# Kernel optimization log

Hardware: AMD Instinct MI355X
Metric: run time of the kernel (lower is better)

The kernel has to match this reference:

```python
import jax, jax.numpy as jnp
import numpy as np

N = 50000
E = 800000
D_IN = 256
D_OUT = 256
ALPHA = 0.5


def setup_inputs() -> dict:
    key = jax.random.key(0)
    k1, k2, k3, k4, k5, k6 = jax.random.split(key, 6)
    stdv = 1.0 / np.sqrt(D_OUT)
    return {
        "input": jax.random.normal(k1, (N, D_IN), dtype=jnp.float32),
        "adj_src": jax.random.randint(k2, (E,), 0, N, dtype=jnp.int64),
        "adj_dst": jax.random.randint(k3, (E,), 0, N, dtype=jnp.int64),
        "adj_w": jax.random.uniform(k4, (E,), dtype=jnp.float32),
        "init_input": jax.random.normal(k5, (N, D_OUT), dtype=jnp.float32),
        "weight": jax.random.uniform(k6, (D_IN, D_OUT), dtype=jnp.float32,
                                     minval=-stdv, maxval=stdv),
    }


def reference(input, adj_src, adj_dst, adj_w, init_input, weight):
    # support = input @ W          [N, D_OUT] (dense GEMM)
    support = jnp.matmul(input, weight)
    # spmm: out[dst] += w * support[src]   (COO aggregate)
    msgs = support[adj_src] * adj_w[:, None]          # [E, D_OUT]
    agg = jax.ops.segment_sum(msgs, adj_dst, num_segments=N)  # [N, D_OUT]
    # alpha-blended residual + ReLU (bias=False, act=ReLU)
    out = agg * ALPHA + init_input * (1.0 - ALPHA)
    return jax.nn.relu(out)
```

## Files before the change

kernel.cpp:

```cpp
#include <hip/hip_runtime.h>
#include <hip/hip_fp16.h>

#define ALPHA 0.5f

typedef short short8v __attribute__((ext_vector_type(8)));
typedef float f32x4 __attribute__((ext_vector_type(4)));

__device__ __forceinline__ unsigned short f2bf(float f) {
  union { float f; unsigned u; } v; v.f = f;
  unsigned r = v.u + 0x7FFFu + ((v.u >> 16) & 1u);
  return (unsigned short)(r >> 16);
}
__device__ __forceinline__ float bf2f(unsigned short u) {
  union { unsigned u; float f; } v; v.u = ((unsigned)u) << 16;
  return v.f;
}

__global__ void transpose_w(const float* __restrict__ W, unsigned short* __restrict__ Wt) {
  __shared__ float tile[16][17];
  int kb = blockIdx.x * 16, nb = blockIdx.y * 16;
  tile[threadIdx.y][threadIdx.x] = W[(kb + threadIdx.y) * 256 + nb + threadIdx.x];
  __syncthreads();
  Wt[(nb + threadIdx.y) * 256 + kb + threadIdx.x] = f2bf(tile[threadIdx.x][threadIdx.y]);
}

__global__ __launch_bounds__(256) void gemm_mfma(
    const float* __restrict__ A, const unsigned short* __restrict__ Wt,
    unsigned short* __restrict__ C, int M) {
  __shared__ char smem[2][24576];
  const int tid = threadIdx.x;
  const int lane = tid & 63;
  const int w = tid >> 6;
  const int wm = w >> 1, wn = w & 1;
  const int row0 = blockIdx.x * 128;

  f32x4 acc[4][8];
  #pragma unroll
  for (int m = 0; m < 4; ++m)
    #pragma unroll
    for (int n = 0; n < 8; ++n) acc[m][n] = (f32x4){0.f, 0.f, 0.f, 0.f};

  const int aR = tid >> 1;
  const int aKs = (tid & 1) * 16;
  const int aRow = (row0 + aR < M) ? (row0 + aR) : (M - 1);
  const float* aP = A + (size_t)aRow * 256 + aKs;
  const int aWrOff = (aR >> 4) * 1024 + (aKs >> 3) * 256 + (aR & 15) * 16;

  int cur = 0;
  {
    float4 av[4];
    #pragma unroll
    for (int j = 0; j < 4; ++j) av[j] = *reinterpret_cast<const float4*>(aP + j * 4);
    #pragma unroll
    for (int i = 0; i < 4; ++i) {
      int s = w * 4 + i;
      const unsigned short* g = Wt + (size_t)(s * 16 + (lane & 15)) * 256 + (lane >> 4) * 8;
      __builtin_amdgcn_global_load_lds(
          (const __attribute__((address_space(1))) void*)g,
          (__attribute__((address_space(3))) void*)(&smem[0][8192 + s * 1024]),
          16, 0, 0);
    }
    unsigned short ab[16];
    #pragma unroll
    for (int j = 0; j < 4; ++j) {
      ab[j * 4 + 0] = f2bf(av[j].x); ab[j * 4 + 1] = f2bf(av[j].y);
      ab[j * 4 + 2] = f2bf(av[j].z); ab[j * 4 + 3] = f2bf(av[j].w);
    }
    *reinterpret_cast<short8v*>(&smem[0][aWrOff])       = *reinterpret_cast<short8v*>(&ab[0]);
    *reinterpret_cast<short8v*>(&smem[0][aWrOff + 256]) = *reinterpret_cast<short8v*>(&ab[8]);
    __syncthreads();
  }

  #pragma unroll
  for (int t = 0; t < 8; ++t) {
    float4 av[4];
    const bool pf = (t < 7);
    if (pf) {
      const int k0 = (t + 1) * 32;
      #pragma unroll
      for (int j = 0; j < 4; ++j) av[j] = *reinterpret_cast<const float4*>(aP + k0 + j * 4);
      #pragma unroll
      for (int i = 0; i < 4; ++i) {
        int s = w * 4 + i;
        const unsigned short* g = Wt + (size_t)(s * 16 + (lane & 15)) * 256 + k0 + (lane >> 4) * 8;
        __builtin_amdgcn_global_load_lds(
            (const __attribute__((address_space(1))) void*)g,
            (__attribute__((address_space(3))) void*)(&smem[cur ^ 1][8192 + s * 1024]),
            16, 0, 0);
      }
    }
    short8v af[4], bfv[8];
    #pragma unroll
    for (int m = 0; m < 4; ++m)
      af[m] = *reinterpret_cast<const short8v*>(&smem[cur][(wm * 4 + m) * 1024 + lane * 16]);
    #pragma unroll
    for (int n = 0; n < 8; ++n)
      bfv[n] = *reinterpret_cast<const short8v*>(&smem[cur][8192 + (wn * 8 + n) * 1024 + lane * 16]);
    #pragma unroll
    for (int m = 0; m < 4; ++m)
      #pragma unroll
      for (int n = 0; n < 8; ++n)
        acc[m][n] = __builtin_amdgcn_mfma_f32_16x16x32_bf16(af[m], bfv[n], acc[m][n], 0, 0, 0);
    if (pf) {
      unsigned short ab[16];
      #pragma unroll
      for (int j = 0; j < 4; ++j) {
        ab[j * 4 + 0] = f2bf(av[j].x); ab[j * 4 + 1] = f2bf(av[j].y);
        ab[j * 4 + 2] = f2bf(av[j].z); ab[j * 4 + 3] = f2bf(av[j].w);
      }
      *reinterpret_cast<short8v*>(&smem[cur ^ 1][aWrOff])       = *reinterpret_cast<short8v*>(&ab[0]);
      *reinterpret_cast<short8v*>(&smem[cur ^ 1][aWrOff + 256]) = *reinterpret_cast<short8v*>(&ab[8]);
    }
    __syncthreads();
    cur ^= 1;
  }

  #pragma unroll
  for (int m = 0; m < 4; ++m) {
    #pragma unroll
    for (int n = 0; n < 8; ++n) {
      const int col = wn * 128 + n * 16 + (lane & 15);
      #pragma unroll
      for (int r = 0; r < 4; ++r) {
        const int row = row0 + wm * 64 + m * 16 + (lane >> 4) * 4 + r;
        if (row < M) C[(size_t)row * 256 + col] = f2bf(acc[m][n][r]);
      }
    }
  }
}

__global__ void histogram_dst(const int* __restrict__ dst, int* __restrict__ deg, int E) {
  int i = blockIdx.x * blockDim.x + threadIdx.x;
  if (i < E) atomicAdd(&deg[dst[i]], 1);
}

__global__ __launch_bounds__(256) void scan_pass1(const int* __restrict__ deg,
                                                  int* __restrict__ excl,
                                                  int* __restrict__ partial, int N) {
  const int tid = threadIdx.x;
  const int base = blockIdx.x * 1024 + tid * 4;
  int4 v = make_int4(0, 0, 0, 0);
  if (base + 3 < N) v = *reinterpret_cast<const int4*>(&deg[base]);
  else {
    if (base + 0 < N) v.x = deg[base + 0];
    if (base + 1 < N) v.y = deg[base + 1];
    if (base + 2 < N) v.z = deg[base + 2];
  }
  const int s = v.x + v.y + v.z + v.w;
  const int lane = tid & 63, wid = tid >> 6;
  int ps = s;
  #pragma unroll
  for (int off = 1; off < 64; off <<= 1) {
    int t = __shfl_up(ps, off, 64);
    if (lane >= off) ps += t;
  }
  __shared__ int wsum[4];
  if (lane == 63) wsum[wid] = ps;
  __syncthreads();
  int woff = 0;
  #pragma unroll
  for (int w2 = 0; w2 < 4; ++w2) woff += (w2 < wid) ? wsum[w2] : 0;
  const int texcl = woff + ps - s;
  int4 e = make_int4(texcl, texcl + v.x, texcl + v.x + v.y, texcl + v.x + v.y + v.z);
  if (base + 3 < N) *reinterpret_cast<int4*>(&excl[base]) = e;
  else {
    if (base + 0 < N) excl[base + 0] = e.x;
    if (base + 1 < N) excl[base + 1] = e.y;
    if (base + 2 < N) excl[base + 2] = e.z;
  }
  if (tid == 255) partial[blockIdx.x] = woff + ps;
}

__global__ __launch_bounds__(256) void scan_pass2(const int* __restrict__ excl,
                                                  const int* __restrict__ partial,
                                                  int* __restrict__ row_ptr,
                                                  int* __restrict__ cursor, int N, int NB) {
  __shared__ int s_off;
  const int tid = threadIdx.x;
  if (tid < 64) {
    int v = (tid < NB && tid < (int)blockIdx.x) ? partial[tid] : 0;
    #pragma unroll
    for (int off = 1; off < 64; off <<= 1) v += __shfl_xor(v, off, 64);
    if (tid == 0) s_off = v;
  }
  __syncthreads();
  const int off = s_off;
  const int base = blockIdx.x * 1024 + tid * 4;
  if (base + 3 < N) {
    int4 v = *reinterpret_cast<const int4*>(&excl[base]);
    v.x += off; v.y += off; v.z += off; v.w += off;
    *reinterpret_cast<int4*>(&row_ptr[base]) = v;
    *reinterpret_cast<int4*>(&cursor[base]) = v;
  } else {
    for (int j = 0; j < 4; ++j)
      if (base + j < N) { int v = excl[base + j] + off; row_ptr[base + j] = v; cursor[base + j] = v; }
  }
}

__global__ void reindex_edges(const int* __restrict__ src, const int* __restrict__ dst,
                              const float* __restrict__ w, int* __restrict__ cursor,
                              unsigned* __restrict__ edges, int E) {
  int i = blockIdx.x * blockDim.x + threadIdx.x;
  if (i < E) {
    int d = dst[i];
    int slot = atomicAdd(&cursor[d], 1);
    unsigned hb = __half_as_ushort(__float2half(w[i] * ALPHA));
    edges[slot] = ((unsigned)src[i] << 15) | (hb >> 1);
  }
}

__device__ __forceinline__ float unpack_w(unsigned p) {
  return __half2float(__ushort_as_half((unsigned short)((p & 0x7FFFu) << 1)));
}

__global__ __launch_bounds__(256) void aggregate(
    const unsigned short* __restrict__ support,
    const int* __restrict__ row_ptr, const int* __restrict__ deg,
    const unsigned* __restrict__ edges,
    const float* __restrict__ init, float* __restrict__ out, int N) {
  int node = blockIdx.x * 4 + (threadIdx.x >> 6);
  if (node >= N) return;
  int lane = threadIdx.x & 63;
  int start = row_ptr[node], cnt = deg[node];

  float4 ini = *reinterpret_cast<const float4*>(&init[(size_t)node * 256 + lane * 4]);

  float4 acc = make_float4(0.f, 0.f, 0.f, 0.f);
  int e = 0;
  for (; e + 7 < cnt; e += 8) {
    unsigned p[8];
    #pragma unroll
    for (int j = 0; j < 8; ++j) p[j] = edges[start + e + j];
    ushort4 v[8];
    #pragma unroll
    for (int j = 0; j < 8; ++j)
      v[j] = *reinterpret_cast<const ushort4*>(&support[(size_t)(p[j] >> 15) * 256 + lane * 4]);
    #pragma unroll
    for (int j = 0; j < 8; ++j) {
      float wj = unpack_w(p[j]);
      acc.x += wj * bf2f(v[j].x);
      acc.y += wj * bf2f(v[j].y);
      acc.z += wj * bf2f(v[j].z);
      acc.w += wj * bf2f(v[j].w);
    }
  }
  for (; e < cnt; ++e) {
    unsigned p = edges[start + e];
    ushort4 v = *reinterpret_cast<const ushort4*>(&support[(size_t)(p >> 15) * 256 + lane * 4]);
    float wj = unpack_w(p);
    acc.x += wj * bf2f(v.x); acc.y += wj * bf2f(v.y);
    acc.z += wj * bf2f(v.z); acc.w += wj * bf2f(v.w);
  }
  float4 o;
  o.x = fmaxf(acc.x + (1.f - ALPHA) * ini.x, 0.f);
  o.y = fmaxf(acc.y + (1.f - ALPHA) * ini.y, 0.f);
  o.z = fmaxf(acc.z + (1.f - ALPHA) * ini.z, 0.f);
  o.w = fmaxf(acc.w + (1.f - ALPHA) * ini.w, 0.f);
  *reinterpret_cast<float4*>(&out[(size_t)node * 256 + lane * 4]) = o;
}

extern "C" void kernel_launch(void* const* d_in, const int* in_sizes, int n_in,
                              void* d_out, int out_size, void* d_ws, size_t ws_size,
                              hipStream_t stream) {
  const float* input   = (const float*)d_in[0];
  const int*   adj_src = (const int*)d_in[1];
  const int*   adj_dst = (const int*)d_in[2];
  const float* adj_w   = (const float*)d_in[3];
  const float* init_in = (const float*)d_in[4];
  const float* weight  = (const float*)d_in[5];
  float* out = (float*)d_out;

  const int N = in_sizes[0] / 256;
  const int E = in_sizes[1];

  char* ws = (char*)d_ws;
  unsigned short* support = (unsigned short*)ws; ws += (size_t)N * 256 * 2;
  unsigned short* Wt      = (unsigned short*)ws; ws += 256 * 256 * 2;
  int* deg     = (int*)ws; ws += (size_t)N * 4;
  int* row_ptr = (int*)ws; ws += (size_t)N * 4;
  int* cursor  = (int*)ws; ws += (size_t)N * 4;
  int* excl    = (int*)ws; ws += (size_t)N * 4;
  int* partial = (int*)ws; ws += 256;
  unsigned* edges = (unsigned*)ws; ws += (size_t)E * 4;

  const int NB = (N + 1023) / 1024;

  transpose_w<<<dim3(16, 16), dim3(16, 16), 0, stream>>>(weight, Wt);
  gemm_mfma<<<dim3((N + 127) / 128), 256, 0, stream>>>(input, Wt, support, N);

  hipMemsetAsync(deg, 0, (size_t)N * 4, stream);
  histogram_dst<<<(E + 255) / 256, 256, 0, stream>>>(adj_dst, deg, E);
  scan_pass1<<<NB, 256, 0, stream>>>(deg, excl, partial, N);
  scan_pass2<<<NB, 256, 0, stream>>>(excl, partial, row_ptr, cursor, N, NB);
  reindex_edges<<<(E + 255) / 256, 256, 0, stream>>>(adj_src, adj_dst, adj_w, cursor, edges, E);

  aggregate<<<(N + 3) / 4, 256, 0, stream>>>(support, row_ptr, deg, edges, init_in, out, N);
}
```

Before: 191.8 us.

## Store support in column slices and split aggregation across eight feature slices

The GEMM now writes support as eight column slices of 32 features each (slice-major layout). Aggregation launches eight times as many blocks, one per slice, with each wavefront's halves handling alternate edges and combining them through a cross-lane shuffle. The aim is to make each slice small enough to fit in cache, so gathers from random source nodes hit L2/MALL more often. In exchange, edge indices are re-read eight times, each gather is a 2-byte scalar load (64 bytes per row) instead of a vector load, half the lanes sit idle at write-out, and the GEMM stores become strided.

```diff
diff --git a/kernel.cpp b/kernel.cpp
--- a/kernel.cpp
+++ b/kernel.cpp
@@ -115,15 +115,18 @@
     cur ^= 1;
   }
 
+  const size_t N32 = (size_t)M * 32;
   #pragma unroll
   for (int m = 0; m < 4; ++m) {
     #pragma unroll
     for (int n = 0; n < 8; ++n) {
       const int col = wn * 128 + n * 16 + (lane & 15);
+      const int slice = col >> 5, cwi = col & 31;
+      unsigned short* cb = C + (size_t)slice * N32 + cwi;
       #pragma unroll
       for (int r = 0; r < 4; ++r) {
         const int row = row0 + wm * 64 + m * 16 + (lane >> 4) * 4 + r;
-        if (row < M) C[(size_t)row * 256 + col] = f2bf(acc[m][n][r]);
+        if (row < M) cb[(size_t)row * 32] = f2bf(acc[m][n][r]);
       }
     }
   }
@@ -218,45 +221,39 @@
     const int* __restrict__ row_ptr, const int* __restrict__ deg,
     const unsigned* __restrict__ edges,
     const float* __restrict__ init, float* __restrict__ out, int N) {
-  int node = blockIdx.x * 4 + (threadIdx.x >> 6);
+  const int slice = blockIdx.x & 7;
+  const int node = (blockIdx.x >> 3) * 4 + (threadIdx.x >> 6);
   if (node >= N) return;
-  int lane = threadIdx.x & 63;
-  int start = row_ptr[node], cnt = deg[node];
-
-  float4 ini = *reinterpret_cast<const float4*>(&init[(size_t)node * 256 + lane * 4]);
-
-  float4 acc = make_float4(0.f, 0.f, 0.f, 0.f);
+  const int lane = threadIdx.x & 63;
+  const int f = lane & 31;
+  const int par = lane >> 5;
+  const unsigned short* sb = support + (size_t)slice * ((size_t)N * 32) + f;
+  const int start = row_ptr[node], cnt = deg[node];
+
+  float acc = 0.f;
   int e = 0;
   for (; e + 7 < cnt; e += 8) {
-    unsigned p[8];
-    #pragma unroll
-    for (int j = 0; j < 8; ++j) p[j] = edges[start + e + j];
-    ushort4 v[8];
-    #pragma unroll
-    for (int j = 0; j < 8; ++j)
-      v[j] = *reinterpret_cast<const ushort4*>(&support[(size_t)(p[j] >> 15) * 256 + lane * 4]);
-    #pragma unroll
-    for (int j = 0; j < 8; ++j) {
-      float wj = unpack_w(p[j]);
-      acc.x += wj * bf2f(v[j].x);
-      acc.y += wj * bf2f(v[j].y);
-      acc.z += wj * bf2f(v[j].z);
-      acc.w += wj * bf2f(v[j].w);
-    }
-  }
-  for (; e < cnt; ++e) {
-    unsigned p = edges[start + e];
-    ushort4 v = *reinterpret_cast<const ushort4*>(&support[(size_t)(p >> 15) * 256 + lane * 4]);
-    float wj = unpack_w(p);
-    acc.x += wj * bf2f(v.x); acc.y += wj * bf2f(v.y);
-    acc.z += wj * bf2f(v.z); acc.w += wj * bf2f(v.w);
-  }
-  float4 o;
-  o.x = fmaxf(acc.x + (1.f - ALPHA) * ini.x, 0.f);
-  o.y = fmaxf(acc.y + (1.f - ALPHA) * ini.y, 0.f);
-  o.z = fmaxf(acc.z + (1.f - ALPHA) * ini.z, 0.f);
-  o.w = fmaxf(acc.w + (1.f - ALPHA) * ini.w, 0.f);
-  *reinterpret_cast<float4*>(&out[(size_t)node * 256 + lane * 4]) = o;
+    unsigned p0 = edges[start + e + 0 + par];
+    unsigned p1 = edges[start + e + 2 + par];
+    unsigned p2 = edges[start + e + 4 + par];
+    unsigned p3 = edges[start + e + 6 + par];
+    unsigned short v0 = sb[(size_t)(p0 >> 15) * 32];
+    unsigned short v1 = sb[(size_t)(p1 >> 15) * 32];
+    unsigned short v2 = sb[(size_t)(p2 >> 15) * 32];
+    unsigned short v3 = sb[(size_t)(p3 >> 15) * 32];
+    acc += unpack_w(p0) * bf2f(v0) + unpack_w(p1) * bf2f(v1)
+         + unpack_w(p2) * bf2f(v2) + unpack_w(p3) * bf2f(v3);
+  }
+  for (; e + par < cnt; e += 2) {
+    unsigned p = edges[start + e + par];
+    acc += unpack_w(p) * bf2f(sb[(size_t)(p >> 15) * 32]);
+  }
+  acc += __shfl_xor(acc, 32, 64);
+  if (par == 0) {
+    const int col = slice * 32 + f;
+    float ini = init[(size_t)node * 256 + col];
+    out[(size_t)node * 256 + col] = fmaxf(acc + (1.f - ALPHA) * ini, 0.f);
+  }
 }
 
 extern "C" void kernel_launch(void* const* d_in, const int* in_sizes, int n_in,
@@ -294,5 +291,5 @@
   scan_pass2<<<NB, 256, 0, stream>>>(excl, partial, row_ptr, cursor, N, NB);
   reindex_edges<<<(E + 255) / 256, 256, 0, stream>>>(adj_src, adj_dst, adj_w, cursor, edges, E);
 
-  aggregate<<<(N + 3) / 4, 256, 0, stream>>>(support, row_ptr, deg, edges, init_in, out, N);
-}
+  aggregate<<<((N + 3) / 4) * 8, 256, 0, stream>>>(support, row_ptr, deg, edges, init_in, out, N);
+}
```

Measured after the change: 294.4 us. +53.5%, slower.

## Fuse histogram into GEMM launch, merge prep kernels, vectorize edge reindex

Applied to the files above, without the earlier changes.

The weight transpose and the degree-buffer zeroing are merged into one small prep kernel, replacing a separate kernel plus a memset. The destination histogram now runs as extra blocks inside the GEMM launch, so its atomics can overlap with the MFMA work instead of running as a serial stage. The edge reindex kernel is vectorized to four edges per thread. Aggregation now takes each node's degree from an N+1 row_ptr array instead of a separate deg read. The changes cut launch count and serialization, at the cost of the histogram blocks competing with GEMM blocks for CUs, and the reindex tail handling assumes E is nearly a multiple of 4.

```diff
diff --git a/kernel.cpp b/kernel.cpp
--- a/kernel.cpp
+++ b/kernel.cpp
@@ -15,24 +15,55 @@
   union { unsigned u; float f; } v; v.u = ((unsigned)u) << 16;
   return v.f;
 }
-
-__global__ void transpose_w(const float* __restrict__ W, unsigned short* __restrict__ Wt) {
-  __shared__ float tile[16][17];
-  int kb = blockIdx.x * 16, nb = blockIdx.y * 16;
-  tile[threadIdx.y][threadIdx.x] = W[(kb + threadIdx.y) * 256 + nb + threadIdx.x];
-  __syncthreads();
-  Wt[(nb + threadIdx.y) * 256 + kb + threadIdx.x] = f2bf(tile[threadIdx.x][threadIdx.y]);
-}
-
-__global__ __launch_bounds__(256) void gemm_mfma(
+__device__ __forceinline__ float unpack_w(unsigned p) {
+  return __half2float(__ushort_as_half((unsigned short)((p & 0x7FFFu) << 1)));
+}
+
+__global__ __launch_bounds__(256) void prep_small(
+    const float* __restrict__ W, unsigned short* __restrict__ Wt,
+    int* __restrict__ deg, int N) {
+  const int tid = threadIdx.x;
+  const int bid = blockIdx.x;
+  if (bid < 256) {
+    __shared__ float tile[16][17];
+    const int kb = (bid & 15) * 16, nb = (bid >> 4) * 16;
+    const int tx = tid & 15, ty = tid >> 4;
+    tile[ty][tx] = W[(kb + ty) * 256 + nb + tx];
+    __syncthreads();
+    Wt[(nb + ty) * 256 + kb + tx] = f2bf(tile[tx][ty]);
+  } else {
+    const int i4 = (bid - 256) * 256 + tid;
+    const int base = i4 * 4;
+    if (base + 3 < N) *reinterpret_cast<int4*>(&deg[base]) = make_int4(0, 0, 0, 0);
+    else for (int j = 0; j < 4; ++j) if (base + j < N) deg[base + j] = 0;
+  }
+}
+
+__global__ __launch_bounds__(256) void gemm_hist(
     const float* __restrict__ A, const unsigned short* __restrict__ Wt,
-    unsigned short* __restrict__ C, int M) {
+    unsigned short* __restrict__ C, int M,
+    const int* __restrict__ dst, int* __restrict__ deg, int E, int GB, int HB) {
   __shared__ char smem[2][24576];
   const int tid = threadIdx.x;
+  const int bid = blockIdx.x;
+
+  if (bid >= GB) {
+    const int hgid = (bid - GB) * 256 + tid;
+    const int hstride = HB * 256;
+    const int E4 = E & ~3;
+    for (int i = hgid * 4; i < E4; i += hstride * 4) {
+      int4 d = *reinterpret_cast<const int4*>(&dst[i]);
+      atomicAdd(&deg[d.x], 1); atomicAdd(&deg[d.y], 1);
+      atomicAdd(&deg[d.z], 1); atomicAdd(&deg[d.w], 1);
+    }
+    if (hgid < (E - E4)) atomicAdd(&deg[dst[E4 + hgid]], 1);
+    return;
+  }
+
   const int lane = tid & 63;
   const int w = tid >> 6;
   const int wm = w >> 1, wn = w & 1;
-  const int row0 = blockIdx.x * 128;
+  const int row0 = bid * 128;
 
   f32x4 acc[4][8];
   #pragma unroll
@@ -127,11 +158,6 @@
       }
     }
   }
-}
-
-__global__ void histogram_dst(const int* __restrict__ dst, int* __restrict__ deg, int E) {
-  int i = blockIdx.x * blockDim.x + threadIdx.x;
-  if (i < E) atomicAdd(&deg[dst[i]], 1);
 }
 
 __global__ __launch_bounds__(256) void scan_pass1(const int* __restrict__ deg,
@@ -174,7 +200,8 @@
 __global__ __launch_bounds__(256) void scan_pass2(const int* __restrict__ excl,
                                                   const int* __restrict__ partial,
                                                   int* __restrict__ row_ptr,
-                                                  int* __restrict__ cursor, int N, int NB) {
+                                                  int* __restrict__ cursor,
+                                                  int N, int NB, int E) {
   __shared__ int s_off;
   const int tid = threadIdx.x;
   if (tid < 64) {
@@ -183,6 +210,7 @@
     for (int off = 1; off < 64; off <<= 1) v += __shfl_xor(v, off, 64);
     if (tid == 0) s_off = v;
   }
+  if (blockIdx.x == 0 && tid == 0) row_ptr[N] = E;
   __syncthreads();
   const int off = s_off;
   const int base = blockIdx.x * 1024 + tid * 4;
@@ -197,31 +225,43 @@
   }
 }
 
-__global__ void reindex_edges(const int* __restrict__ src, const int* __restrict__ dst,
-                              const float* __restrict__ w, int* __restrict__ cursor,
-                              unsigned* __restrict__ edges, int E) {
-  int i = blockIdx.x * blockDim.x + threadIdx.x;
-  if (i < E) {
-    int d = dst[i];
-    int slot = atomicAdd(&cursor[d], 1);
-    unsigned hb = __half_as_ushort(__float2half(w[i] * ALPHA));
-    edges[slot] = ((unsigned)src[i] << 15) | (hb >> 1);
-  }
-}
-
-__device__ __forceinline__ float unpack_w(unsigned p) {
-  return __half2float(__ushort_as_half((unsigned short)((p & 0x7FFFu) << 1)));
+__global__ __launch_bounds__(256) void reindex_edges(
+    const int* __restrict__ src, const int* __restrict__ dst,
+    const float* __restrict__ w, int* __restrict__ cursor,
+    unsigned* __restrict__ edges, int E) {
+  int i = (blockIdx.x * blockDim.x + threadIdx.x) * 4;
+  if (i + 3 < E) {
+    int4 sv = *reinterpret_cast<const int4*>(&src[i]);
+    int4 dv = *reinterpret_cast<const int4*>(&dst[i]);
+    float4 wv = *reinterpret_cast<const float4*>(&w[i]);
+    int s_[4] = {sv.x, sv.y, sv.z, sv.w};
+    int d_[4] = {dv.x, dv.y, dv.z, dv.w};
+    float w_[4] = {wv.x, wv.y, wv.z, wv.w};
+    #pragma unroll
+    for (int j = 0; j < 4; ++j) {
+      int slot = atomicAdd(&cursor[d_[j]], 1);
+      unsigned hb = __half_as_ushort(__float2half(w_[j] * ALPHA));
+      edges[slot] = ((unsigned)s_[j] << 15) | (hb >> 1);
+    }
+  } else {
+    for (; i < E; ++i) {
+      int slot = atomicAdd(&cursor[dst[i]], 1);
+      unsigned hb = __half_as_ushort(__float2half(w[i] * ALPHA));
+      edges[slot] = ((unsigned)src[i] << 15) | (hb >> 1);
+    }
+  }
 }
 
 __global__ __launch_bounds__(256) void aggregate(
     const unsigned short* __restrict__ support,
-    const int* __restrict__ row_ptr, const int* __restrict__ deg,
+    const int* __restrict__ row_ptr,
     const unsigned* __restrict__ edges,
     const float* __restrict__ init, float* __restrict__ out, int N) {
   int node = blockIdx.x * 4 + (threadIdx.x >> 6);
   if (node >= N) return;
   int lane = threadIdx.x & 63;
-  int start = row_ptr[node], cnt = deg[node];
+  int start = row_ptr[node];
+  int cnt = row_ptr[node + 1] - start;
 
   float4 ini = *reinterpret_cast<const float4*>(&init[(size_t)node * 256 + lane * 4]);
 
@@ -277,22 +317,24 @@
   unsigned short* support = (unsigned short*)ws; ws += (size_t)N * 256 * 2;
   unsigned short* Wt      = (unsigned short*)ws; ws += 256 * 256 * 2;
   int* deg     = (int*)ws; ws += (size_t)N * 4;
-  int* row_ptr = (int*)ws; ws += (size_t)N * 4;
+  int* row_ptr = (int*)ws; ws += (size_t)(N + 1) * 4;
   int* cursor  = (int*)ws; ws += (size_t)N * 4;
   int* excl    = (int*)ws; ws += (size_t)N * 4;
   int* partial = (int*)ws; ws += 256;
   unsigned* edges = (unsigned*)ws; ws += (size_t)E * 4;
 
   const int NB = (N + 1023) / 1024;
-
-  transpose_w<<<dim3(16, 16), dim3(16, 16), 0, stream>>>(weight, Wt);
-  gemm_mfma<<<dim3((N + 127) / 128), 256, 0, stream>>>(input, Wt, support, N);
-
-  hipMemsetAsync(deg, 0, (size_t)N * 4, stream);
-  histogram_dst<<<(E + 255) / 256, 256, 0, stream>>>(adj_dst, deg, E);
+  const int GB = (N + 127) / 128;
+  const int HB = 800;
+
+  prep_small<<<256 + (N / 4 + 255) / 256, 256, 0, stream>>>(weight, Wt, deg, N);
+
+  gemm_hist<<<GB + HB, 256, 0, stream>>>(input, Wt, support, N,
+                                         adj_dst, deg, E, GB, HB);
+
   scan_pass1<<<NB, 256, 0, stream>>>(deg, excl, partial, N);
-  scan_pass2<<<NB, 256, 0, stream>>>(excl, partial, row_ptr, cursor, N, NB);
-  reindex_edges<<<(E + 255) / 256, 256, 0, stream>>>(adj_src, adj_dst, adj_w, cursor, edges, E);
-
-  aggregate<<<(N + 3) / 4, 256, 0, stream>>>(support, row_ptr, deg, edges, init_in, out, N);
-}
+  scan_pass2<<<NB, 256, 0, stream>>>(excl, partial, row_ptr, cursor, N, NB, E);
+  reindex_edges<<<(E / 4 + 255) / 256, 256, 0, stream>>>(adj_src, adj_dst, adj_w, cursor, edges, E);
+
+  aggregate<<<(N + 3) / 4, 256, 0, stream>>>(support, row_ptr, edges, init_in, out, N);
+}
```

New measurement: 173.2 us. 9.7% less time.
